# Optimization experiments

Measured on AMD Instinct MI355X. Metric: run time of the kernel, lower is better.

The kernel has to match this reference:

```python
import jax, jax.numpy as jnp
import numpy as np

COMMITMENT_COST = 0.25


def setup_inputs() -> dict:
    key = jax.random.key(0)
    k1, k2 = jax.random.split(key)
    inputs = jax.random.normal(k1, (32, 512, 32, 32), dtype=jnp.float32)
    embeddings = jax.random.normal(k2, (4096, 512), dtype=jnp.float32)
    return {"inputs": inputs, "embeddings": embeddings}


def reference(inputs, embeddings):
    # NCHW -> NHWC, flatten to (N, D)
    x = jnp.transpose(inputs, (0, 2, 3, 1))  # [B,H,W,D]
    D = embeddings.shape[1]
    z = x.reshape(-1, D)  # [N,D]

    # Squared L2 distances: ||z||^2 - 2 z E^T + ||E||^2
    d1 = jnp.sum(z * z, axis=1, keepdims=True)            # [N,1]
    d2 = 2.0 * jnp.matmul(z, embeddings.T)                # [N,K]
    d3 = jnp.sum(embeddings * embeddings, axis=1)[None]   # [1,K]
    distances = d1 - d2 + d3                              # [N,K]

    k = jnp.argmin(distances, axis=1)                     # [N]
    q = embeddings[k]                                     # [N,D] gather

    # latent loss: codebook loss + commitment loss
    e_loss = jnp.mean((jax.lax.stop_gradient(z) - q) ** 2)
    q_loss = COMMITMENT_COST * jnp.mean((z - jax.lax.stop_gradient(q)) ** 2)
    loss = e_loss + q_loss

    qx = q.reshape(x.shape)                               # [B,H,W,D]
    output = jnp.transpose(qx, (0, 3, 1, 2))              # NCHW
    return output, loss
```

## Files before the change

kernel.cpp:

```cpp
#include <hip/hip_runtime.h>

#define N_PTS 32768
#define DIM   512
#define KCODES 4096
#define HW    1024
#define MARGIN 0.125f
#define MAXFLAG 2048

typedef _Float16 half8 __attribute__((ext_vector_type(8)));
typedef float f32x4 __attribute__((ext_vector_type(4)));
typedef unsigned long long u64;

#define E16_OFF   0
#define BIAS_OFF  4194304
#define TOP2_OFF  4210688
#define ZC_OFF    5259264


__device__ __forceinline__ unsigned mono(float f) {
    unsigned u = __float_as_uint(f);
    return (u & 0x80000000u) ? ~u : (u | 0x80000000u);
}
__device__ __forceinline__ float unmono(unsigned m) {
    unsigned u = (m & 0x80000000u) ? (m & 0x7FFFFFFFu) : ~m;
    return __uint_as_float(u);
}

#define ASYNC16(src, dst) __builtin_amdgcn_global_load_lds( \
    (const __attribute__((address_space(1))) void*)(src), \
    (__attribute__((address_space(3))) void*)(dst), 16, 0, 0)

__global__ void prep_e_kernel(const float* __restrict__ E, _Float16* __restrict__ E16,
                              float* __restrict__ bias) {
    int k = blockIdx.x;
    int l = threadIdx.x;
    const float4* row = (const float4*)(E + (size_t)k * DIM);
    float4 a = row[l * 2];
    float4 b = row[l * 2 + 1];
    half8 h;
    h[0] = (_Float16)a.x; h[1] = (_Float16)a.y; h[2] = (_Float16)a.z; h[3] = (_Float16)a.w;
    h[4] = (_Float16)b.x; h[5] = (_Float16)b.y; h[6] = (_Float16)b.z; h[7] = (_Float16)b.w;
    *(half8*)(E16 + (size_t)k * DIM + l * 8) = h;
    float s = a.x * a.x + a.y * a.y + a.z * a.z + a.w * a.w +
              b.x * b.x + b.y * b.y + b.z * b.z + b.w * b.w;
#pragma unroll
    for (int off = 32; off > 0; off >>= 1) s += __shfl_down(s, off, 64);
    if (l == 0) bias[k] = 0.5f * s;
}

__global__ __launch_bounds__(512, 2) void score16_kernel(
    const float* __restrict__ in, const _Float16* __restrict__ E16,
    const float* __restrict__ bias, u64* __restrict__ top2)
{
    __shared__ alignas(16) _Float16 stage[3][16384];
    __shared__ alignas(16) float bias_sm[2048];

    const int t    = threadIdx.x;
    const int lane = t & 63;
    const int w    = t >> 6;
    const int lm   = lane & 15;
    const int lq   = lane >> 4;
    const int ks   = blockIdx.x;
    const int pt0  = blockIdx.y * 256;

    half8 zf[2][16];
#pragma unroll
    for (int pt = 0; pt < 2; pt++) {
        const int n = pt0 + 32 * w + 16 * pt + lm;
        const float* zb = in + (size_t)(n >> 10) * (DIM * HW) + (n & 1023);
#pragma unroll
        for (int kc = 0; kc < 16; kc++) {
            const int d0 = kc * 32 + lq * 8;
            half8 h;
#pragma unroll
            for (int j = 0; j < 8; j++) h[j] = (_Float16)zb[(size_t)(d0 + j) << 10];
            zf[pt][kc] = h;
        }
    }
    asm volatile("s_waitcnt vmcnt(0)" ::: "memory");

    ASYNC16(bias + ks * 2048 + w * 256 + lane * 4, &bias_sm[w * 256]);

    auto stage_half = [&](int b, int fn, int hn) {
        const int cn = ks * 2048 + (fn & 31) * 64;
#pragma unroll
        for (int i = 0; i < 4; i++) {
            ASYNC16(E16 + (size_t)(cn + i * 16 + lm) * DIM + hn * 256 + w * 32 + lq * 8,
                    &stage[b][(size_t)(w * 4 + i) << 9]);
        }
    };

    stage_half(0, 0, 0);
    stage_half(1, 0, 1);

    const u64 PKNEG = ((u64)0x007FFFFFu) << 32;
    u64 b1[2], b2[2];
    float thr2[2];
#pragma unroll
    for (int p = 0; p < 2; p++) { b1[p] = PKNEG; b2[p] = PKNEG; thr2[p] = -INFINITY; }

    for (int f = 0; f < 32; f++) {
        const int code0 = ks * 2048 + f * 64;
        const int bA = (2 * f) % 3;
        const int bB = (2 * f + 1) % 3;

        f32x4 acc[4][2];

        asm volatile("s_waitcnt vmcnt(4)" ::: "memory");
        __builtin_amdgcn_s_barrier();
        asm volatile("" ::: "memory");
        stage_half((2 * f + 2) % 3, f + 1, 0);
#pragma unroll
        for (int ct = 0; ct < 4; ct++) {
            const float4 bv = *(const float4*)&bias_sm[f * 64 + ct * 16 + lq * 4];
            f32x4 bi; bi[0] = -bv.x; bi[1] = -bv.y; bi[2] = -bv.z; bi[3] = -bv.w;
            acc[ct][0] = bi; acc[ct][1] = bi;
        }
#pragma unroll
        for (int kc = 0; kc < 8; kc++) {
#pragma unroll
            for (int ct = 0; ct < 4; ct++) {
                half8 a = *(const half8*)&stage[bA][(size_t)((kc * 4 + ct) * 512 + lane * 8)];
                acc[ct][0] = __builtin_amdgcn_mfma_f32_16x16x32_f16(a, zf[0][kc], acc[ct][0], 0, 0, 0);
                acc[ct][1] = __builtin_amdgcn_mfma_f32_16x16x32_f16(a, zf[1][kc], acc[ct][1], 0, 0, 0);
            }
        }
        asm volatile("s_waitcnt lgkmcnt(0)" ::: "memory");

        asm volatile("s_waitcnt vmcnt(4)" ::: "memory");
        __builtin_amdgcn_s_barrier();
        asm volatile("" ::: "memory");
        stage_half((2 * f + 3) % 3, f + 1, 1);
#pragma unroll
        for (int kc = 0; kc < 8; kc++) {
#pragma unroll
            for (int ct = 0; ct < 4; ct++) {
                half8 a = *(const half8*)&stage[bB][(size_t)((kc * 4 + ct) * 512 + lane * 8)];
                acc[ct][0] = __builtin_amdgcn_mfma_f32_16x16x32_f16(a, zf[0][8 + kc], acc[ct][0], 0, 0, 0);
                acc[ct][1] = __builtin_amdgcn_mfma_f32_16x16x32_f16(a, zf[1][8 + kc], acc[ct][1], 0, 0, 0);
            }
        }
#pragma unroll
        for (int pt = 0; pt < 2; pt++) {
#pragma unroll
            for (int ct = 0; ct < 4; ct++) {
                f32x4 a = acc[ct][pt];
                bool hit = (a[0] > thr2[pt]) | (a[1] > thr2[pt]) |
                           (a[2] > thr2[pt]) | (a[3] > thr2[pt]);
                if (__any(hit)) {
#pragma unroll
                    for (int r = 0; r < 4; r++) {
                        float v = a[r];
                        if (v > thr2[pt]) {
                            int code = code0 + ct * 16 + lq * 4 + r;
                            u64 pk = ((u64)mono(v) << 32) | (unsigned)(0xFFFu ^ (unsigned)code);
                            if (pk > b1[pt]) { b2[pt] = b1[pt]; b1[pt] = pk; }
                            else if (pk > b2[pt]) { b2[pt] = pk; }
                            thr2[pt] = unmono((unsigned)(b2[pt] >> 32));
                        }
                    }
                }
            }
        }
        asm volatile("s_waitcnt lgkmcnt(0)" ::: "memory");
    }
    asm volatile("s_waitcnt vmcnt(0)" ::: "memory");

#pragma unroll
    for (int pt = 0; pt < 2; pt++) {
#pragma unroll
        for (int m = 16; m <= 32; m <<= 1) {
            u64 o1 = __shfl_xor(b1[pt], m, 64);
            u64 o2 = __shfl_xor(b2[pt], m, 64);
            u64 m1 = b1[pt] > o1 ? b1[pt] : o1;
            u64 lo = b1[pt] > o1 ? o1 : b1[pt];
            u64 mm = b2[pt] > o2 ? b2[pt] : o2;
            b2[pt] = lo > mm ? lo : mm;
            b1[pt] = m1;
        }
    }
    if (lq == 0) {
#pragma unroll
        for (int pt = 0; pt < 2; pt++) {
            const size_t p = (size_t)(pt0 + 32 * w + 16 * pt + lm);
            top2[p * 4 + ks * 2]     = b1[pt];
            top2[p * 4 + ks * 2 + 1] = b2[pt];
        }
    }
}

__global__ void merge_compact_kernel(const u64* __restrict__ top2, const float* __restrict__ in,
                                     int* __restrict__ k_final, int* __restrict__ list,
                                     int* __restrict__ count, float* __restrict__ zc) {
    int pt = blockIdx.x * 256 + threadIdx.x;
    const u64* p = top2 + (size_t)pt * 4;
    u64 B1 = 0, B2 = 0;
#pragma unroll
    for (int ks = 0; ks < 2; ks++) {
        u64 p1 = p[ks * 2], p2 = p[ks * 2 + 1];
        u64 m1 = B1 > p1 ? B1 : p1;
        u64 lo = B1 > p1 ? p1 : B1;
        u64 mm = B2 > p2 ? B2 : p2;
        B2 = lo > mm ? lo : mm;
        B1 = m1;
    }
    k_final[pt] = 0xFFF ^ (int)(B1 & 0xFFFull);
    float s1 = unmono((unsigned)(B1 >> 32));
    float s2 = unmono((unsigned)(B2 >> 32));
    if (s1 - s2 < MARGIN) {
        int idx = atomicAdd(count, 1);
        if (idx < MAXFLAG) {
            list[idx] = pt;
            const float* zb = in + (size_t)(pt >> 10) * (DIM * HW) + (pt & 1023);
            float* dst = zc + (size_t)idx * DIM;
#pragma unroll 8
            for (int d = 0; d < DIM; d++) dst[d] = zb[(size_t)d << 10];
        }
    }
}

__global__ __launch_bounds__(256) void rescore_kernel(
    const float* __restrict__ zc, const float* __restrict__ E,
    const float* __restrict__ bias, const int* __restrict__ count,
    u64* __restrict__ rb)
{
    __shared__ float As[16][128];
    __shared__ float Bs[16][132];

    int cnt = *count; if (cnt > MAXFLAG) cnt = MAXFLAG;
    const int t  = threadIdx.x;
    const int k0 = blockIdx.x * 128;
    const int r0 = blockIdx.y * 128;
    if (r0 >= cnt) return;

    float acc[8][8];
#pragma unroll
    for (int i = 0; i < 8; i++)
#pragma unroll
        for (int j = 0; j < 8; j++) acc[i][j] = 0.f;

    const int ra = (t >> 4) << 2;
    const int cb = (t & 15) << 2;

    for (int d0 = 0; d0 < DIM; d0 += 16) {
        {
            int j   = t >> 2;
            int dd4 = (t & 3) << 2;
            int rA = r0 + j;        if (rA >= cnt) rA = cnt - 1;
            int rB = r0 + j + 64;   if (rB >= cnt) rB = cnt - 1;
            float4 v0 = *(const float4*)&zc[(size_t)rA * DIM + d0 + dd4];
            float4 v1 = *(const float4*)&zc[(size_t)rB * DIM + d0 + dd4];
            As[dd4 + 0][j] = v0.x; As[dd4 + 1][j] = v0.y;
            As[dd4 + 2][j] = v0.z; As[dd4 + 3][j] = v0.w;
            As[dd4 + 0][j + 64] = v1.x; As[dd4 + 1][j + 64] = v1.y;
            As[dd4 + 2][j + 64] = v1.z; As[dd4 + 3][j + 64] = v1.w;
        }
        {
            int j   = t >> 2;
            int dd4 = (t & 3) << 2;
            const float* p = E + (size_t)(k0 + j) * DIM + d0 + dd4;
            float4 v0 = *(const float4*)p;
            float4 v1 = *(const float4*)(p + (size_t)64 * DIM);
            Bs[dd4 + 0][j] = v0.x; Bs[dd4 + 1][j] = v0.y;
            Bs[dd4 + 2][j] = v0.z; Bs[dd4 + 3][j] = v0.w;
            Bs[dd4 + 0][j + 64] = v1.x; Bs[dd4 + 1][j + 64] = v1.y;
            Bs[dd4 + 2][j + 64] = v1.z; Bs[dd4 + 3][j + 64] = v1.w;
        }
        __syncthreads();
#pragma unroll
        for (int dd = 0; dd < 16; dd++) {
            float4 a0 = *(const float4*)&As[dd][ra];
            float4 a1 = *(const float4*)&As[dd][ra + 64];
            float4 b0 = *(const float4*)&Bs[dd][cb];
            float4 b1v = *(const float4*)&Bs[dd][cb + 64];
            float av[8] = {a0.x, a0.y, a0.z, a0.w, a1.x, a1.y, a1.z, a1.w};
            float bv[8] = {b0.x, b0.y, b0.z, b0.w, b1v.x, b1v.y, b1v.z, b1v.w};
#pragma unroll
            for (int i = 0; i < 8; i++)
#pragma unroll
                for (int j = 0; j < 8; j++)
                    acc[i][j] = fmaf(av[i], bv[j], acc[i][j]);
        }
        __syncthreads();
    }

    float bcol[8];
#pragma unroll
    for (int j = 0; j < 8; j++) {
        int k = k0 + ((j < 4) ? (cb + j) : (64 + cb + j - 4));
        bcol[j] = bias[k];
    }
    u64 pk[8];
#pragma unroll
    for (int i = 0; i < 8; i++) {
        u64 bestp = 0ull;
#pragma unroll
        for (int j = 0; j < 8; j++) {
            int k = k0 + ((j < 4) ? (cb + j) : (64 + cb + j - 4));
            float s = acc[i][j] - bcol[j];
            u64 p = ((u64)mono(s) << 32) | (u64)(~(unsigned)k);
            if (p > bestp) bestp = p;
        }
        pk[i] = bestp;
    }
#pragma unroll
    for (int i = 0; i < 8; i++) {
#pragma unroll
        for (int off = 8; off > 0; off >>= 1) {
            u64 o = __shfl_down(pk[i], off, 16);
            if (o > pk[i]) pk[i] = o;
        }
    }
    if ((t & 15) == 0) {
#pragma unroll
        for (int i = 0; i < 8; i++) {
            int row = r0 + ((i < 4) ? (ra + i) : (64 + ra + i - 4));
            int slot = row < cnt ? row : cnt - 1;
            atomicMax(&rb[slot], pk[i]);
        }
    }
}

__global__ void apply_kernel(const int* __restrict__ list, const int* __restrict__ count,
                             const u64* __restrict__ rb, int* __restrict__ k_final) {
    int i = blockIdx.x * 256 + threadIdx.x;
    int cnt = *count; if (cnt > MAXFLAG) cnt = MAXFLAG;
    if (i < cnt) k_final[list[i]] = (int)(~(unsigned)(rb[i] & 0xffffffffull));
}

__global__ void gather_kernel(const float* __restrict__ in, const float* __restrict__ E,
                              const int* __restrict__ k_final,
                              float* __restrict__ out, float* __restrict__ sumsq)
{
    const int t  = threadIdx.x;
    const int tx = t & 63;
    const int ty = t >> 6;
    const int n  = blockIdx.x * 64 + tx;
    const int k  = k_final[n];
    const float* erow = E + (size_t)k * DIM;
    const size_t base = (size_t)(n >> 10) * (DIM * HW) + (n & 1023);
    float local = 0.f;
    for (int d = ty; d < DIM; d += 4) {
        float q = erow[d];
        size_t idx = base + ((size_t)d << 10);
        float z = in[idx];
        out[idx] = q;
        float df = z - q;
        local = fmaf(df, df, local);
    }
#pragma unroll
    for (int off = 32; off > 0; off >>= 1) local += __shfl_down(local, off, 64);
    __shared__ float red[4];
    if (tx == 0) red[ty] = local;
    __syncthreads();
    if (t == 0) atomicAdd(sumsq, red[0] + red[1] + red[2] + red[3]);
}

__global__ void finalize_kernel(const float* __restrict__ sumsq, float* __restrict__ out_loss) {
    *out_loss = 1.25f * (*sumsq) * (1.0f / 16777216.0f);
}

extern "C" void kernel_launch(void* const* d_in, const int* in_sizes, int n_in,
                              void* d_out, int out_size, void* d_ws, size_t ws_size,
                              hipStream_t stream) {
    const float* in = (const float*)d_in[0];
    const float* E  = (const float*)d_in[1];
    float* out = (float*)d_out;
    char* ob = (char*)d_out;

    _Float16* E16 = (_Float16*)(ob + E16_OFF);
    float* bias   = (float*)(ob + BIAS_OFF);
    u64* top2     = (u64*)(ob + TOP2_OFF);
    float* zc     = (float*)(ob + ZC_OFF);

    u64* rb      = (u64*)d_ws;
    int* count   = (int*)((char*)d_ws + 16384);
    float* sumsq = (float*)((char*)d_ws + 16388);
    int* list    = (int*)((char*)d_ws + 16392);
    int* k_final = (int*)((char*)d_ws + 24584);

    hipMemsetAsync(d_ws, 0, 16392, stream);

    prep_e_kernel<<<KCODES, 64, 0, stream>>>(E, E16, bias);

    score16_kernel<<<dim3(2, 128), 512, 0, stream>>>(in, E16, bias, top2);

    merge_compact_kernel<<<128, 256, 0, stream>>>(top2, in, k_final, list, count, zc);

    rescore_kernel<<<dim3(32, 16), 256, 0, stream>>>(zc, E, bias, count, rb);
    apply_kernel<<<8, 256, 0, stream>>>(list, count, rb, k_final);

    gather_kernel<<<N_PTS / 64, 256, 0, stream>>>(in, E, k_final, out, sumsq);
    finalize_kernel<<<1, 1, 0, stream>>>(sumsq, out + 16777216);
}
```

Baseline: 512.8 us.

## Pre-transpose inputs to fp16 and retile scoring GEMM with LDS-staged 2D tiles

Adds a prep kernel that transposes the NCHW input into a row-major fp16 z matrix, so z no longer has to be loaded with strided per-element reads inside the scoring kernel. The scoring kernel becomes a conventional 2D-tiled GEMM: each block covers 256 points by 1024 codes, and z and E tiles are staged through LDS with triple buffering. Each wave computes an 8x4 grid of MFMA tiles to increase operand reuse, and partial top-2 results are merged in LDS. This costs an extra pass over the input plus an intermediate fp16 buffer, and the epilogue now merges four partial top-2 results per point.

```diff
diff --git a/kernel.cpp b/kernel.cpp
--- a/kernel.cpp
+++ b/kernel.cpp
@@ -14,7 +14,8 @@
 #define E16_OFF   0
 #define BIAS_OFF  4194304
 #define TOP2_OFF  4210688
-#define ZC_OFF    5259264
+#define ZC_OFF    6307840
+#define Z16_OFF   10502144
 
 
 __device__ __forceinline__ unsigned mono(float f) {
@@ -48,144 +49,181 @@
     if (l == 0) bias[k] = 0.5f * s;
 }
 
-__global__ __launch_bounds__(512, 2) void score16_kernel(
-    const float* __restrict__ in, const _Float16* __restrict__ E16,
-    const float* __restrict__ bias, u64* __restrict__ top2)
+__global__ __launch_bounds__(256) void prep_z_kernel(const float* __restrict__ in,
+                                                     _Float16* __restrict__ z16) {
+    __shared__ _Float16 tile[64 * 520];
+    const int t  = threadIdx.x;
+    const int hw0 = blockIdx.x * 64;
+    const int b   = blockIdx.y;
+    const float* src = in + (size_t)b * (DIM * HW) + hw0;
+    const int hl = t & 63, dq = t >> 6;
+    for (int i = 0; i < 128; i++) {
+        int d = i * 4 + dq;
+        tile[hl * 520 + d] = (_Float16)src[((size_t)d << 10) + hl];
+    }
+    __syncthreads();
+    const size_t zbase = (size_t)(b * 1024 + hw0) * DIM;
+    const int w = t >> 6, L = t & 63;
+#pragma unroll
+    for (int k = 0; k < 16; k++) {
+        int g = k * 256 + t;
+        half8 v = *(const half8*)((const char*)tile + (size_t)(k * 4 + w) * 1040 + L * 16);
+        *(half8*)(z16 + zbase + (size_t)g * 8) = v;
+    }
+}
+
+__global__ __launch_bounds__(512, 2) void score_gemm_kernel(
+    const _Float16* __restrict__ z16, const _Float16* __restrict__ E16,
+    const float* __restrict__ bias, u64* __restrict__ top2p)
 {
-    __shared__ alignas(16) _Float16 stage[3][16384];
-    __shared__ alignas(16) float bias_sm[2048];
+    __shared__ alignas(16) _Float16 Ab[3][8192];
+    __shared__ alignas(16) _Float16 Eb[3][8192];
+    __shared__ u64 mrg[4][256][2];
 
     const int t    = threadIdx.x;
     const int lane = t & 63;
     const int w    = t >> 6;
     const int lm   = lane & 15;
     const int lq   = lane >> 4;
-    const int ks   = blockIdx.x;
+    const int wr   = w >> 2;
+    const int wc   = w & 3;
+    const int Nb   = blockIdx.x;
     const int pt0  = blockIdx.y * 256;
 
-    half8 zf[2][16];
-#pragma unroll
-    for (int pt = 0; pt < 2; pt++) {
-        const int n = pt0 + 32 * w + 16 * pt + lm;
-        const float* zb = in + (size_t)(n >> 10) * (DIM * HW) + (n & 1023);
-#pragma unroll
-        for (int kc = 0; kc < 16; kc++) {
-            const int d0 = kc * 32 + lq * 8;
-            half8 h;
-#pragma unroll
-            for (int j = 0; j < 8; j++) h[j] = (_Float16)zb[(size_t)(d0 + j) << 10];
-            zf[pt][kc] = h;
-        }
-    }
-    asm volatile("s_waitcnt vmcnt(0)" ::: "memory");
-
-    ASYNC16(bias + ks * 2048 + w * 256 + lane * 4, &bias_sm[w * 256]);
-
-    auto stage_half = [&](int b, int fn, int hn) {
-        const int cn = ks * 2048 + (fn & 31) * 64;
-#pragma unroll
-        for (int i = 0; i < 4; i++) {
-            ASYNC16(E16 + (size_t)(cn + i * 16 + lm) * DIM + hn * 256 + w * 32 + lq * 8,
-                    &stage[b][(size_t)(w * 4 + i) << 9]);
-        }
-    };
-
-    stage_half(0, 0, 0);
-    stage_half(1, 0, 1);
+    {
+        u64* m = &mrg[0][0][0];
+        for (int i = t; i < 2048; i += 512) m[i] = 0;
+    }
+    __syncthreads();
 
     const u64 PKNEG = ((u64)0x007FFFFFu) << 32;
-    u64 b1[2], b2[2];
-    float thr2[2];
-#pragma unroll
-    for (int p = 0; p < 2; p++) { b1[p] = PKNEG; b2[p] = PKNEG; thr2[p] = -INFINITY; }
-
-    for (int f = 0; f < 32; f++) {
-        const int code0 = ks * 2048 + f * 64;
-        const int bA = (2 * f) % 3;
-        const int bB = (2 * f + 1) % 3;
-
-        f32x4 acc[4][2];
-
-        asm volatile("s_waitcnt vmcnt(4)" ::: "memory");
+
+    for (int np = 0; np < 4; np++) {
+        const int code0 = Nb * 1024 + np * 256;
+
+        float4 bv[4];
+#pragma unroll
+        for (int ci = 0; ci < 4; ci++)
+            bv[ci] = *(const float4*)&bias[code0 + wc * 64 + ci * 16 + lq * 4];
+
+        auto stage_step = [&](int s) {
+            const int bb = s % 3;
+            const int d0 = s * 32;
+#pragma unroll
+            for (int j = 0; j < 2; j++) {
+                const int P = 2 * w + j;
+                ASYNC16(z16 + (size_t)(pt0 + P * 16 + lm) * DIM + d0 + lq * 8,
+                        &Ab[bb][P * 512]);
+            }
+#pragma unroll
+            for (int j = 0; j < 2; j++) {
+                const int C = 2 * w + j;
+                ASYNC16(E16 + (size_t)(code0 + C * 16 + lm) * DIM + d0 + lq * 8,
+                        &Eb[bb][C * 512]);
+            }
+        };
+        stage_step(0);
+        stage_step(1);
+
+        f32x4 acc[8][4];
+#pragma unroll
+        for (int ci = 0; ci < 4; ci++) {
+            f32x4 bi; bi[0] = -bv[ci].x; bi[1] = -bv[ci].y; bi[2] = -bv[ci].z; bi[3] = -bv[ci].w;
+#pragma unroll
+            for (int pi = 0; pi < 8; pi++) acc[pi][ci] = bi;
+        }
+
+        for (int ks = 0; ks < 16; ks++) {
+            if (ks < 15) { asm volatile("s_waitcnt vmcnt(4)" ::: "memory"); }
+            else         { asm volatile("s_waitcnt vmcnt(0)" ::: "memory"); }
+            __builtin_amdgcn_s_barrier();
+            asm volatile("" ::: "memory");
+            if (ks < 14) stage_step(ks + 2);
+            const int bb = ks % 3;
+            half8 bfrag[8], afrag[4];
+#pragma unroll
+            for (int pi = 0; pi < 8; pi++)
+                bfrag[pi] = *(const half8*)&Ab[bb][(wr * 8 + pi) * 512 + lane * 8];
+#pragma unroll
+            for (int ci = 0; ci < 4; ci++)
+                afrag[ci] = *(const half8*)&Eb[bb][(wc * 4 + ci) * 512 + lane * 8];
+#pragma unroll
+            for (int pi = 0; pi < 8; pi++)
+#pragma unroll
+                for (int ci = 0; ci < 4; ci++)
+                    acc[pi][ci] = __builtin_amdgcn_mfma_f32_16x16x32_f16(
+                        afrag[ci], bfrag[pi], acc[pi][ci], 0, 0, 0);
+            asm volatile("s_waitcnt lgkmcnt(0)" ::: "memory");
+        }
         __builtin_amdgcn_s_barrier();
         asm volatile("" ::: "memory");
-        stage_half((2 * f + 2) % 3, f + 1, 0);
-#pragma unroll
-        for (int ct = 0; ct < 4; ct++) {
-            const float4 bv = *(const float4*)&bias_sm[f * 64 + ct * 16 + lq * 4];
-            f32x4 bi; bi[0] = -bv.x; bi[1] = -bv.y; bi[2] = -bv.z; bi[3] = -bv.w;
-            acc[ct][0] = bi; acc[ct][1] = bi;
-        }
-#pragma unroll
-        for (int kc = 0; kc < 8; kc++) {
-#pragma unroll
-            for (int ct = 0; ct < 4; ct++) {
-                half8 a = *(const half8*)&stage[bA][(size_t)((kc * 4 + ct) * 512 + lane * 8)];
-                acc[ct][0] = __builtin_amdgcn_mfma_f32_16x16x32_f16(a, zf[0][kc], acc[ct][0], 0, 0, 0);
-                acc[ct][1] = __builtin_amdgcn_mfma_f32_16x16x32_f16(a, zf[1][kc], acc[ct][1], 0, 0, 0);
-            }
-        }
-        asm volatile("s_waitcnt lgkmcnt(0)" ::: "memory");
-
-        asm volatile("s_waitcnt vmcnt(4)" ::: "memory");
-        __builtin_amdgcn_s_barrier();
-        asm volatile("" ::: "memory");
-        stage_half((2 * f + 3) % 3, f + 1, 1);
-#pragma unroll
-        for (int kc = 0; kc < 8; kc++) {
-#pragma unroll
-            for (int ct = 0; ct < 4; ct++) {
-                half8 a = *(const half8*)&stage[bB][(size_t)((kc * 4 + ct) * 512 + lane * 8)];
-                acc[ct][0] = __builtin_amdgcn_mfma_f32_16x16x32_f16(a, zf[0][8 + kc], acc[ct][0], 0, 0, 0);
-                acc[ct][1] = __builtin_amdgcn_mfma_f32_16x16x32_f16(a, zf[1][8 + kc], acc[ct][1], 0, 0, 0);
-            }
-        }
-#pragma unroll
-        for (int pt = 0; pt < 2; pt++) {
-#pragma unroll
-            for (int ct = 0; ct < 4; ct++) {
-                f32x4 a = acc[ct][pt];
-                bool hit = (a[0] > thr2[pt]) | (a[1] > thr2[pt]) |
-                           (a[2] > thr2[pt]) | (a[3] > thr2[pt]);
+
+        u64 pb1[8], pb2[8];
+#pragma unroll
+        for (int pi = 0; pi < 8; pi++) { pb1[pi] = PKNEG; pb2[pi] = PKNEG; }
+#pragma unroll
+        for (int pi = 0; pi < 8; pi++) {
+            float thr = -INFINITY;
+#pragma unroll
+            for (int ci = 0; ci < 4; ci++) {
+                f32x4 a = acc[pi][ci];
+                bool hit = (a[0] > thr) | (a[1] > thr) | (a[2] > thr) | (a[3] > thr);
                 if (__any(hit)) {
 #pragma unroll
                     for (int r = 0; r < 4; r++) {
                         float v = a[r];
-                        if (v > thr2[pt]) {
-                            int code = code0 + ct * 16 + lq * 4 + r;
+                        if (v > thr) {
+                            int code = code0 + wc * 64 + ci * 16 + lq * 4 + r;
                             u64 pk = ((u64)mono(v) << 32) | (unsigned)(0xFFFu ^ (unsigned)code);
-                            if (pk > b1[pt]) { b2[pt] = b1[pt]; b1[pt] = pk; }
-                            else if (pk > b2[pt]) { b2[pt] = pk; }
-                            thr2[pt] = unmono((unsigned)(b2[pt] >> 32));
+                            if (pk > pb1[pi]) { pb2[pi] = pb1[pi]; pb1[pi] = pk; }
+                            else if (pk > pb2[pi]) { pb2[pi] = pk; }
+                            thr = unmono((unsigned)(pb2[pi] >> 32));
                         }
                     }
                 }
             }
         }
-        asm volatile("s_waitcnt lgkmcnt(0)" ::: "memory");
-    }
-    asm volatile("s_waitcnt vmcnt(0)" ::: "memory");
-
-#pragma unroll
-    for (int pt = 0; pt < 2; pt++) {
-#pragma unroll
-        for (int m = 16; m <= 32; m <<= 1) {
-            u64 o1 = __shfl_xor(b1[pt], m, 64);
-            u64 o2 = __shfl_xor(b2[pt], m, 64);
-            u64 m1 = b1[pt] > o1 ? b1[pt] : o1;
-            u64 lo = b1[pt] > o1 ? o1 : b1[pt];
-            u64 mm = b2[pt] > o2 ? b2[pt] : o2;
-            b2[pt] = lo > mm ? lo : mm;
-            b1[pt] = m1;
-        }
-    }
-    if (lq == 0) {
-#pragma unroll
-        for (int pt = 0; pt < 2; pt++) {
-            const size_t p = (size_t)(pt0 + 32 * w + 16 * pt + lm);
-            top2[p * 4 + ks * 2]     = b1[pt];
-            top2[p * 4 + ks * 2 + 1] = b2[pt];
-        }
+#pragma unroll
+        for (int pi = 0; pi < 8; pi++) {
+#pragma unroll
+            for (int m = 16; m <= 32; m <<= 1) {
+                u64 o1 = __shfl_xor(pb1[pi], m, 64);
+                u64 o2 = __shfl_xor(pb2[pi], m, 64);
+                u64 m1 = pb1[pi] > o1 ? pb1[pi] : o1;
+                u64 lo = pb1[pi] > o1 ? o1 : pb1[pi];
+                u64 mm = pb2[pi] > o2 ? pb2[pi] : o2;
+                pb2[pi] = lo > mm ? lo : mm;
+                pb1[pi] = m1;
+            }
+        }
+        if (lq == 0) {
+#pragma unroll
+            for (int pi = 0; pi < 8; pi++) {
+                const int ptl = wr * 128 + pi * 16 + lm;
+                u64 c1 = mrg[wc][ptl][0], c2 = mrg[wc][ptl][1];
+                u64 m1 = c1 > pb1[pi] ? c1 : pb1[pi];
+                u64 lo = c1 > pb1[pi] ? pb1[pi] : c1;
+                u64 mm = c2 > pb2[pi] ? c2 : pb2[pi];
+                mrg[wc][ptl][0] = m1;
+                mrg[wc][ptl][1] = lo > mm ? lo : mm;
+            }
+        }
+    }
+
+    __syncthreads();
+    if (t < 256) {
+        u64 B1 = 0, B2 = 0;
+#pragma unroll
+        for (int s = 0; s < 4; s++) {
+            u64 p1 = mrg[s][t][0], p2 = mrg[s][t][1];
+            u64 m1 = B1 > p1 ? B1 : p1;
+            u64 lo = B1 > p1 ? p1 : B1;
+            u64 mm = B2 > p2 ? B2 : p2;
+            B2 = lo > mm ? lo : mm;
+            B1 = m1;
+        }
+        u64* dst = top2p + (size_t)(pt0 + t) * 8 + Nb * 2;
+        dst[0] = B1; dst[1] = B2;
     }
 }
 
@@ -193,11 +231,11 @@
                                      int* __restrict__ k_final, int* __restrict__ list,
                                      int* __restrict__ count, float* __restrict__ zc) {
     int pt = blockIdx.x * 256 + threadIdx.x;
-    const u64* p = top2 + (size_t)pt * 4;
+    const u64* p = top2 + (size_t)pt * 8;
     u64 B1 = 0, B2 = 0;
 #pragma unroll
-    for (int ks = 0; ks < 2; ks++) {
-        u64 p1 = p[ks * 2], p2 = p[ks * 2 + 1];
+    for (int s = 0; s < 4; s++) {
+        u64 p1 = p[s * 2], p2 = p[s * 2 + 1];
         u64 m1 = B1 > p1 ? B1 : p1;
         u64 lo = B1 > p1 ? p1 : B1;
         u64 mm = B2 > p2 ? B2 : p2;
@@ -370,8 +408,9 @@
 
     _Float16* E16 = (_Float16*)(ob + E16_OFF);
     float* bias   = (float*)(ob + BIAS_OFF);
-    u64* top2     = (u64*)(ob + TOP2_OFF);
+    u64* top2p    = (u64*)(ob + TOP2_OFF);
     float* zc     = (float*)(ob + ZC_OFF);
+    _Float16* z16 = (_Float16*)(ob + Z16_OFF);
 
     u64* rb      = (u64*)d_ws;
     int* count   = (int*)((char*)d_ws + 16384);
@@ -382,10 +421,11 @@
     hipMemsetAsync(d_ws, 0, 16392, stream);
 
     prep_e_kernel<<<KCODES, 64, 0, stream>>>(E, E16, bias);
-
-    score16_kernel<<<dim3(2, 128), 512, 0, stream>>>(in, E16, bias, top2);
-
-    merge_compact_kernel<<<128, 256, 0, stream>>>(top2, in, k_final, list, count, zc);
+    prep_z_kernel<<<dim3(16, 32), 256, 0, stream>>>(in, z16);
+
+    score_gemm_kernel<<<dim3(4, 128), 512, 0, stream>>>(z16, E16, bias, top2p);
+
+    merge_compact_kernel<<<128, 256, 0, stream>>>(top2p, in, k_final, list, count, zc);
 
     rescore_kernel<<<dim3(32, 16), 256, 0, stream>>>(zc, E, bias, count, rb);
     apply_kernel<<<8, 256, 0, stream>>>(list, count, rb, k_final);
```

New measurement: 641.0 us. +25.0%, slower.
